# Optimization experiments

Hardware: AMD Instinct MI355X
Metric: run time of the kernel (lower is better)

The kernel has to match this reference:

```python
import jax, jax.numpy as jnp
import numpy as np

B, PS, ENC = 64, 14, 2048
DEC, ATT, EMB = 512, 512, 512
V, L = 10000, 52


def setup_inputs() -> dict:
    key = jax.random.key(0)
    ks = jax.random.split(key, 24)
    rn = lambda k, shp, s=0.02: (jax.random.normal(k, shp) * s).astype(jnp.float32)
    lengths = jax.random.randint(ks[2], (B, 1), 2, L + 1)
    lengths = lengths.at[0, 0].set(L)  # ensure max(decode_lengths) == L-1 (static)
    return {
        "encoder_output": jax.random.normal(ks[0], (B, PS, PS, ENC), jnp.float32),
        "encoded_captions": jax.random.randint(ks[1], (B, L), 0, V),
        "caption_lengths": lengths,
        # embedding (torch init: uniform(-0.1, 0.1))
        "emb_W": jax.random.uniform(ks[3], (V, EMB), jnp.float32, -0.1, 0.1),
        # attention linears
        "att_enc_W": rn(ks[4], (ENC, ATT)), "att_enc_b": jnp.zeros((ATT,), jnp.float32),
        "att_dec_W": rn(ks[5], (DEC, ATT)), "att_dec_b": jnp.zeros((ATT,), jnp.float32),
        "att_full_w": rn(ks[6], (ATT,)), "att_full_b": jnp.zeros((), jnp.float32),
        # LSTMCell(input = EMB + ENC, hidden = DEC)
        "lstm_Wih": rn(ks[7], (4 * DEC, EMB + ENC)), "lstm_Whh": rn(ks[8], (4 * DEC, DEC)),
        "lstm_bih": jnp.zeros((4 * DEC,), jnp.float32), "lstm_bhh": jnp.zeros((4 * DEC,), jnp.float32),
        # init_h / init_c / f_beta / fc
        "initH_W": rn(ks[9], (ENC, DEC)), "initH_b": jnp.zeros((DEC,), jnp.float32),
        "initC_W": rn(ks[10], (ENC, DEC)), "initC_b": jnp.zeros((DEC,), jnp.float32),
        "fbeta_W": rn(ks[11], (DEC, ENC)), "fbeta_b": jnp.zeros((ENC,), jnp.float32),
        "fc_W": jax.random.uniform(ks[12], (DEC, V), jnp.float32, -0.1, 0.1),
        "fc_b": jnp.zeros((V,), jnp.float32),
    }


def reference(encoder_output, encoded_captions, caption_lengths,
              emb_W, att_enc_W, att_enc_b, att_dec_W, att_dec_b,
              att_full_w, att_full_b, lstm_Wih, lstm_Whh, lstm_bih, lstm_bhh,
              initH_W, initH_b, initC_W, initC_b, fbeta_W, fbeta_b, fc_W, fc_b):
    b = encoder_output.shape[0]
    lengths = caption_lengths[:, 0]
    order = jnp.argsort(-lengths)                     # sort descending (sort_idx)
    lengths = lengths[order]
    enc = encoder_output.reshape(b, -1, ENC)[order]   # [B, P, ENC]
    caps = encoded_captions[order]                    # [B, L]
    emb = emb_W[caps]                                 # [B, L, EMB]
    dec_len = lengths - 1                             # decode lengths
    T = caps.shape[1] - 1                             # static max(decode_lengths)

    mean_enc = enc.mean(axis=1)
    h0 = mean_enc @ initH_W + initH_b
    c0 = mean_enc @ initC_W + initC_b
    # precompute encoder half of the attention MLP once
    att1 = jnp.einsum('bpe,ea->bpa', enc, att_enc_W) + att_enc_b  # [B, P, ATT]

    def step(carry, t):
        h, c = carry
        mask = (t < dec_len)[:, None]                 # rows still decoding
        att2 = h @ att_dec_W + att_dec_b              # [B, ATT]
        e = jax.nn.relu(att1 + att2[:, None, :]) @ att_full_w + att_full_b  # [B, P]
        alpha = jax.nn.softmax(e, axis=-1)
        awe = jnp.einsum('bp,bpe->be', alpha, enc)    # attention-weighted encoding
        gate = jax.nn.sigmoid(h @ fbeta_W + fbeta_b)
        x = jnp.concatenate([emb[:, t, :], gate * awe], axis=1)
        gates = x @ lstm_Wih.T + lstm_bih + h @ lstm_Whh.T + lstm_bhh
        i, f, g, o = jnp.split(gates, 4, axis=1)
        c_new = jax.nn.sigmoid(f) * c + jax.nn.sigmoid(i) * jnp.tanh(g)
        h_new = jax.nn.sigmoid(o) * jnp.tanh(c_new)
        pred = h_new @ fc_W + fc_b                    # dropout p=0 -> identity
        h = jnp.where(mask, h_new, h)
        c = jnp.where(mask, c_new, c)
        return (h, c), (jnp.where(mask, pred, 0.0), jnp.where(mask, alpha, 0.0))

    _, (preds, alphas) = jax.lax.scan(step, (h0, c0), jnp.arange(T))
    preds = jnp.transpose(preds, (1, 0, 2))           # [B, T, V]
    alphas = jnp.transpose(alphas, (1, 0, 2))         # [B, T, P]
    return preds, caps, dec_len, alphas, order
```

## Files before the change

### kernel.cpp

```cpp
#include <hip/hip_runtime.h>
#include <math.h>

#define BATCH 64
#define PIX   196
#define ENCD  2048
#define DECD  512
#define ATTD  512
#define EMBD  512
#define VOC   10000
#define LCAP  52
#define TSTEPS 51
#define XHDIM 3072

typedef __bf16 bfv8 __attribute__((ext_vector_type(8)));
typedef float  fv4  __attribute__((ext_vector_type(4)));

__device__ __forceinline__ float bf2f(unsigned short u) {
    union { unsigned int i; float f; } x; x.i = ((unsigned int)u) << 16; return x.f;
}
__device__ __forceinline__ unsigned short f2bf(float f) {
    union { float f; unsigned int i; } x; x.f = f;
    unsigned int r = x.i + 0x7fffu + ((x.i >> 16) & 1u);
    return (unsigned short)(r >> 16);
}

__global__ void k_setup(const int* caps, const int* lens,
                        int* order, int* declen,
                        float* caps_out, float* declen_out, float* order_out) {
    __shared__ int sl[64];
    __shared__ int so[64];
    int tid = threadIdx.x;
    sl[tid] = lens[tid];
    __syncthreads();
    int li = sl[tid];
    int pos = 0;
    for (int j = 0; j < 64; ++j) {
        int lj = sl[j];
        if (lj > li || (lj == li && j < tid)) pos++;
    }
    so[pos] = tid;
    __syncthreads();
    int ob = so[tid];
    order[tid] = ob;
    int dl = sl[ob] - 1;
    declen[tid] = dl;
    order_out[tid] = (float)ob;
    declen_out[tid] = (float)dl;
    for (int l = 0; l < LCAP; ++l)
        caps_out[tid * LCAP + l] = (float)caps[ob * LCAP + l];
}

__global__ void k_emb_all(const float* embW, const int* caps, const int* order,
                          unsigned short* emb_all, unsigned short* xh) {
    int b = blockIdx.x, t = blockIdx.y, tid = threadIdx.x;
    int tok = caps[order[b] * LCAP + t];
    float4 v = *(const float4*)(embW + (size_t)tok * EMBD + tid * 4);
    ushort4 o;
    o.x = f2bf(v.x); o.y = f2bf(v.y); o.z = f2bf(v.z); o.w = f2bf(v.w);
    *(ushort4*)(emb_all + ((size_t)t * 64 + b) * EMBD + tid * 4) = o;
    if (t == 0)
        *(ushort4*)(xh + (size_t)b * XHDIM + tid * 4) = o;
}

__global__ __launch_bounds__(256) void k_cvt_T(const float* src, unsigned short* dst,
                                               int R, int C) {
    __shared__ float tile[64][65];
    int c0 = blockIdx.x * 64, r0 = blockIdx.y * 64, tid = threadIdx.x;
    for (int idx = tid; idx < 4096; idx += 256) {
        int r = idx >> 6, c = idx & 63;
        float v = 0.f;
        if (r0 + r < R && c0 + c < C) v = src[(size_t)(r0 + r) * C + c0 + c];
        tile[r][c] = v;
    }
    __syncthreads();
    for (int idx = tid; idx < 4096; idx += 256) {
        int c = idx >> 6, r = idx & 63;
        if (c0 + c < C && r0 + r < R)
            dst[(size_t)(c0 + c) * R + r0 + r] = f2bf(tile[r][c]);
    }
}

__global__ void k_cvt_comb(const float* Wih, const float* Whh, unsigned short* W) {
    int j = blockIdx.x, tid = threadIdx.x;
    for (int k = tid * 4; k < XHDIM; k += 1024) {
        const float* src = (k < 2560) ? (Wih + (size_t)j * 2560 + k)
                                      : (Whh + (size_t)j * 512 + (k - 2560));
        float4 v = *(const float4*)src;
        ushort4 o;
        o.x = f2bf(v.x); o.y = f2bf(v.y); o.z = f2bf(v.z); o.w = f2bf(v.w);
        *(ushort4*)(W + (size_t)j * XHDIM + k) = o;
    }
}

__global__ void k_cvt_enc(const float* enc, const int* order, unsigned short* enc_bf) {
    int b = blockIdx.x, p = blockIdx.y, tid = threadIdx.x;
    const float* src = enc + ((size_t)order[b] * PIX + p) * ENCD + tid * 8;
    float4 v0 = *(const float4*)src;
    float4 v1 = *(const float4*)(src + 4);
    unsigned short o[8];
    o[0] = f2bf(v0.x); o[1] = f2bf(v0.y); o[2] = f2bf(v0.z); o[3] = f2bf(v0.w);
    o[4] = f2bf(v1.x); o[5] = f2bf(v1.y); o[6] = f2bf(v1.z); o[7] = f2bf(v1.w);
    *(uint4*)(enc_bf + ((size_t)b * PIX + p) * ENCD + tid * 8) = *(uint4*)o;
}

__global__ void k_mean(const float* enc, const int* order, float* meanv) {
    int b = blockIdx.x;
    int col = blockIdx.y * 256 + threadIdx.x;
    int ob = order[b];
    const float* base = enc + (size_t)ob * PIX * ENCD + col;
    float acc = 0.f;
    for (int p = 0; p < PIX; ++p) acc += base[(size_t)p * ENCD];
    meanv[b * ENCD + col] = acc * (1.0f / (float)PIX);
}

__global__ __launch_bounds__(256) void k_h0c0(const float* meanv,
                                              const float* WH, const float* bH,
                                              const float* WC, const float* bC,
                                              float* h, float* c, unsigned short* xh) {
    __shared__ float As[64 * 33];
    __shared__ float Bs[32 * 65];
    int nt = blockIdx.x, tid = threadIdx.x;
    const float* W; const float* bias; float* out; int j0; bool isH;
    if (nt < 8) { W = WH; bias = bH; out = h; j0 = nt * 64; isH = true; }
    else        { W = WC; bias = bC; out = c; j0 = (nt - 8) * 64; isH = false; }
    float acc[4][4] = {};
    int tr = tid & 15, tc = tid >> 4;
    for (int k0 = 0; k0 < ENCD; k0 += 32) {
        for (int idx = tid; idx < 512; idx += 256) {
            int rl = idx >> 3, k4 = (idx & 7) << 2;
            float4 v = *(const float4*)(meanv + (size_t)rl * ENCD + k0 + k4);
            float* d = As + rl * 33 + k4;
            d[0] = v.x; d[1] = v.y; d[2] = v.z; d[3] = v.w;
        }
        for (int idx = tid; idx < 512; idx += 256) {
            int k = idx >> 4, j4 = (idx & 15) << 2;
            float4 v = *(const float4*)(W + (size_t)(k0 + k) * DECD + j0 + j4);
            float* d = Bs + k * 65 + j4;
            d[0] = v.x; d[1] = v.y; d[2] = v.z; d[3] = v.w;
        }
        __syncthreads();
        for (int kk = 0; kk < 32; ++kk) {
            float a[4], bb[4];
            for (int i = 0; i < 4; ++i) a[i] = As[(tr * 4 + i) * 33 + kk];
            for (int i = 0; i < 4; ++i) bb[i] = Bs[kk * 65 + tc * 4 + i];
            for (int i = 0; i < 4; ++i)
                for (int j2 = 0; j2 < 4; ++j2) acc[i][j2] += a[i] * bb[j2];
        }
        __syncthreads();
    }
    for (int i = 0; i < 4; ++i)
        for (int j2 = 0; j2 < 4; ++j2) {
            int r = tr * 4 + i, j = j0 + tc * 4 + j2;
            float v = acc[i][j2] + bias[j];
            out[r * DECD + j] = v;
            if (isH) xh[(size_t)r * XHDIM + 2560 + j] = f2bf(v);
        }
}

__device__ __forceinline__ void mm64_core(
    const unsigned short* __restrict__ A, int lda,
    const unsigned short* __restrict__ Bt, int ldb,
    int K, int nvalid,
    unsigned short* __restrict__ As, unsigned short* __restrict__ Bs,
    fv4* __restrict__ acc)
{
    const int tid = threadIdx.x;
    const int lane = tid & 63;
    const int w = tid >> 6, wr = w >> 1, wc = w & 1;
    const int lr = lane & 15, lk = (lane >> 4) << 3;
    const int sr = tid >> 2, sc = (tid & 3) << 3;
    const unsigned short* ap = A + (size_t)sr * lda + sc;
    const unsigned short* bp = Bt + (size_t)sr * ldb + sc;
    const bool bok = sr < nvalid;
    unsigned short* aw = As + sr * 40 + sc;
    unsigned short* bw = Bs + sr * 40 + sc;
    const unsigned short* a0p = As + (wr * 32 + lr) * 40 + lk;
    const unsigned short* a1p = a0p + 16 * 40;
    const unsigned short* b0p = Bs + (wc * 32 + lr) * 40 + lk;
    const unsigned short* b1p = b0p + 16 * 40;

    uint4 av = *(const uint4*)ap;
    uint4 bv;
    if (bok) bv = *(const uint4*)bp; else { bv.x = bv.y = bv.z = bv.w = 0u; }

    for (int k0 = 0; k0 < K; k0 += 32) {
        __syncthreads();
        *(uint4*)aw = av;
        *(uint4*)bw = bv;
        if (k0 + 32 < K) {
            av = *(const uint4*)(ap + k0 + 32);
            if (bok) bv = *(const uint4*)(bp + k0 + 32);
            else { bv.x = bv.y = bv.z = bv.w = 0u; }
        }
        __syncthreads();
        bfv8 a0 = *(const bfv8*)a0p;
        bfv8 a1 = *(const bfv8*)a1p;
        bfv8 b0 = *(const bfv8*)b0p;
        bfv8 b1 = *(const bfv8*)b1p;
        acc[0] = __builtin_amdgcn_mfma_f32_16x16x32_bf16(a0, b0, acc[0], 0, 0, 0);
        acc[1] = __builtin_amdgcn_mfma_f32_16x16x32_bf16(a0, b1, acc[1], 0, 0, 0);
        acc[2] = __builtin_amdgcn_mfma_f32_16x16x32_bf16(a1, b0, acc[2], 0, 0, 0);
        acc[3] = __builtin_amdgcn_mfma_f32_16x16x32_bf16(a1, b1, acc[3], 0, 0, 0);
    }
}

#define MM64_DECL_EPI \
    int lane = threadIdx.x & 63; int w = threadIdx.x >> 6; \
    int wr = w >> 1, wc = w & 1; \
    int rg = (lane >> 4) << 2, cg = lane & 15;

__global__ __launch_bounds__(256) void k_att1_mfma(
    const unsigned short* __restrict__ enc_bf, const unsigned short* __restrict__ WaeT,
    const float* __restrict__ bias, unsigned short* __restrict__ att1bf) {
    __shared__ __align__(16) unsigned short As[64 * 40];
    __shared__ __align__(16) unsigned short Bs[64 * 40];
    int r0 = blockIdx.x * 64, a0 = blockIdx.y * 64;
    fv4 acc[4];
    acc[0] = (fv4)0.f; acc[1] = (fv4)0.f; acc[2] = (fv4)0.f; acc[3] = (fv4)0.f;
    mm64_core(enc_bf + (size_t)r0 * ENCD, ENCD,
              WaeT + (size_t)a0 * ENCD, ENCD, ENCD, 64, As, Bs, acc);
    MM64_DECL_EPI
    #pragma unroll
    for (int m = 0; m < 2; ++m)
      #pragma unroll
      for (int n = 0; n < 2; ++n)
        #pragma unroll
        for (int r = 0; r < 4; ++r) {
            int row = r0 + wr * 32 + m * 16 + rg + r;
            int col = a0 + wc * 32 + n * 16 + cg;
            att1bf[(size_t)row * ATTD + col] = f2bf(acc[m * 2 + n][r] + bias[col]);
        }
}

__global__ __launch_bounds__(256) void k_att2gate_mfma(
    const unsigned short* __restrict__ xh, const unsigned short* __restrict__ W2T,
    const float* __restrict__ bad, const float* __restrict__ bfb,
    float* __restrict__ att2, float* __restrict__ gate) {
    __shared__ __align__(16) unsigned short As[64 * 40];
    __shared__ __align__(16) unsigned short Bs[64 * 40];
    int j0 = blockIdx.x * 64;
    fv4 acc[4];
    acc[0] = (fv4)0.f; acc[1] = (fv4)0.f; acc[2] = (fv4)0.f; acc[3] = (fv4)0.f;
    mm64_core(xh + 2560, XHDIM, W2T + (size_t)j0 * DECD, DECD, DECD, 64, As, Bs, acc);
    MM64_DECL_EPI
    #pragma unroll
    for (int m = 0; m < 2; ++m)
      #pragma unroll
      for (int n = 0; n < 2; ++n)
        #pragma unroll
        for (int r = 0; r < 4; ++r) {
            int row = wr * 32 + m * 16 + rg + r;
            int jg = j0 + wc * 32 + n * 16 + cg;
            float v = acc[m * 2 + n][r];
            if (jg < ATTD) {
                att2[row * ATTD + jg] = v + bad[jg];
            } else {
                int jj = jg - ATTD;
                gate[row * ENCD + jj] = 1.f / (1.f + expf(-(v + bfb[jj])));
            }
        }
}

__global__ __launch_bounds__(256) void k_gates_mfma(
    const unsigned short* __restrict__ xh, const unsigned short* __restrict__ W,
    float* __restrict__ partial) {
    __shared__ __align__(16) unsigned short As[64 * 40];
    __shared__ __align__(16) unsigned short Bs[64 * 40];
    int jt = blockIdx.x, kc = blockIdx.y;
    fv4 acc[4];
    acc[0] = (fv4)0.f; acc[1] = (fv4)0.f; acc[2] = (fv4)0.f; acc[3] = (fv4)0.f;
    mm64_core(xh + kc * 512, XHDIM,
              W + (size_t)jt * 64 * XHDIM + kc * 512, XHDIM, 512, 64, As, Bs, acc);
    float* out = partial + (size_t)kc * (64 * 2048);
    MM64_DECL_EPI
    #pragma unroll
    for (int m = 0; m < 2; ++m)
      #pragma unroll
      for (int n = 0; n < 2; ++n)
        #pragma unroll
        for (int r = 0; r < 4; ++r) {
            int row = wr * 32 + m * 16 + rg + r;
            int col = jt * 64 + wc * 32 + n * 16 + cg;
            out[row * 2048 + col] = acc[m * 2 + n][r];
        }
}

__global__ __launch_bounds__(256) void k_fc_mfma(
    const unsigned short* __restrict__ hallbf, const unsigned short* __restrict__ WfcT,
    const float* __restrict__ bias, const int* __restrict__ declen,
    float* __restrict__ preds) {
    __shared__ __align__(16) unsigned short As[64 * 40];
    __shared__ __align__(16) unsigned short Bs[64 * 40];
    int v0 = blockIdx.x * 64, tt = blockIdx.y;
    int nv = VOC - v0; if (nv > 64) nv = 64;
    fv4 acc[4];
    acc[0] = (fv4)0.f; acc[1] = (fv4)0.f; acc[2] = (fv4)0.f; acc[3] = (fv4)0.f;
    mm64_core(hallbf + (size_t)tt * 64 * DECD, DECD,
              WfcT + (size_t)v0 * DECD, DECD, DECD, nv, As, Bs, acc);
    MM64_DECL_EPI
    #pragma unroll
    for (int m = 0; m < 2; ++m)
      #pragma unroll
      for (int n = 0; n < 2; ++n)
        #pragma unroll
        for (int r = 0; r < 4; ++r) {
            int b = wr * 32 + m * 16 + rg + r;
            int v = v0 + wc * 32 + n * 16 + cg;
            if (v < VOC) {
                bool mask = tt < declen[b];
                preds[((size_t)b * TSTEPS + tt) * VOC + v] =
                    mask ? (acc[m * 2 + n][r] + bias[v]) : 0.f;
            }
        }
}

__global__ void k_e(const unsigned short* att1bf, const float* att2,
                    const float* wfull, const float* bfull, float* e) {
    __shared__ float a2s[512];
    __shared__ float wfs[512];
    int b = blockIdx.x, tid = threadIdx.x;
    a2s[tid] = att2[b * ATTD + tid];
    a2s[tid + 256] = att2[b * ATTD + tid + 256];
    wfs[tid] = wfull[tid];
    wfs[tid + 256] = wfull[tid + 256];
    __syncthreads();
    int p = blockIdx.y * 4 + (tid >> 6);
    int lane = tid & 63;
    uint4 v = *(const uint4*)(att1bf + ((size_t)b * PIX + p) * ATTD + lane * 8);
    const unsigned short* us = (const unsigned short*)&v;
    float acc = 0.f;
    for (int jj = 0; jj < 8; ++jj) {
        int a = lane * 8 + jj;
        float x = bf2f(us[jj]) + a2s[a];
        x = fmaxf(x, 0.f);
        acc += x * wfs[a];
    }
    for (int off = 32; off; off >>= 1) acc += __shfl_down(acc, off);
    if (lane == 0) e[b * PIX + p] = acc + bfull[0];
}

__global__ void k_awe(const float* e, const unsigned short* enc_bf,
                      const float* gate, const int* declen,
                      unsigned short* xh, float* alphas_out, int t) {
    __shared__ float sal[256];
    __shared__ float sred[256];
    __shared__ float sacc[2048];
    int b = blockIdx.x, ch = blockIdx.y, tid = threadIdx.x;
    float ev = (tid < PIX) ? e[b * PIX + tid] : -1e30f;
    sred[tid] = ev; __syncthreads();
    for (int s = 128; s; s >>= 1) { if (tid < s) sred[tid] = fmaxf(sred[tid], sred[tid + s]); __syncthreads(); }
    float m = sred[0]; __syncthreads();
    float pv = (tid < PIX) ? expf(ev - m) : 0.f;
    sred[tid] = pv; __syncthreads();
    for (int s = 128; s; s >>= 1) { if (tid < s) sred[tid] += sred[tid + s]; __syncthreads(); }
    float inv = 1.f / sred[0];
    float al = pv * inv;
    sal[tid] = al;
    if (ch == 0 && tid < PIX) {
        bool mask = t < declen[b];
        alphas_out[((size_t)b * TSTEPS + t) * PIX + tid] = mask ? al : 0.f;
    }
    __syncthreads();
    int g = tid & 31, pp = tid >> 5;
    float acc[8] = {};
    const unsigned short* base = enc_bf + (size_t)b * PIX * ENCD + ch * 256 + g * 8;
    for (int p = pp; p < PIX; p += 8) {
        uint4 v = *(const uint4*)(base + (size_t)p * ENCD);
        const unsigned short* us = (const unsigned short*)&v;
        float a = sal[p];
        for (int jj = 0; jj < 8; ++jj) acc[jj] += a * bf2f(us[jj]);
    }
    for (int jj = 0; jj < 8; ++jj) sacc[pp * 256 + g * 8 + jj] = acc[jj];
    __syncthreads();
    float s = 0.f;
    for (int q = 0; q < 8; ++q) s += sacc[q * 256 + tid];
    int col = ch * 256 + tid;
    xh[(size_t)b * XHDIM + EMBD + col] = f2bf(gate[b * ENCD + col] * s);
}

__global__ void k_update(const float* partial, const float* bih, const float* bhh,
                         const int* declen, float* h, float* c,
                         unsigned short* hallbf, const unsigned short* emb_all,
                         unsigned short* xh, int t) {
    int b = blockIdx.x, d = threadIdx.x;
    float g[4];
    for (int q = 0; q < 4; ++q) {
        int j = q * 512 + d;
        float acc = bih[j] + bhh[j];
        for (int kc = 0; kc < 6; ++kc) acc += partial[(size_t)kc * 131072 + b * 2048 + j];
        g[q] = acc;
    }
    float si = 1.f / (1.f + expf(-g[0]));
    float sf = 1.f / (1.f + expf(-g[1]));
    float gg = tanhf(g[2]);
    float so = 1.f / (1.f + expf(-g[3]));
    float c_old = c[b * DECD + d], h_old = h[b * DECD + d];
    float c_new = sf * c_old + si * gg;
    float h_new = so * tanhf(c_new);
    bool mask = t < declen[b];
    float h_keep = mask ? h_new : h_old;
    h[b * DECD + d] = h_keep;
    c[b * DECD + d] = mask ? c_new : c_old;
    xh[(size_t)b * XHDIM + 2560 + d] = f2bf(h_keep);
    hallbf[((size_t)t * 64 + b) * DECD + d] = f2bf(h_new);
    if (t + 1 < TSTEPS)
        xh[(size_t)b * XHDIM + d] = emb_all[((size_t)(t + 1) * 64 + b) * EMBD + d];
}

extern "C" void kernel_launch(void* const* d_in, const int* in_sizes, int n_in,
                              void* d_out, int out_size, void* d_ws, size_t ws_size,
                              hipStream_t stream) {
    const float* enc      = (const float*)d_in[0];
    const int*   caps     = (const int*)d_in[1];
    const int*   lens     = (const int*)d_in[2];
    const float* embW     = (const float*)d_in[3];
    const float* att_enc_W = (const float*)d_in[4];
    const float* att_enc_b = (const float*)d_in[5];
    const float* att_dec_W = (const float*)d_in[6];
    const float* att_dec_b = (const float*)d_in[7];
    const float* att_full_w = (const float*)d_in[8];
    const float* att_full_b = (const float*)d_in[9];
    const float* lstm_Wih = (const float*)d_in[10];
    const float* lstm_Whh = (const float*)d_in[11];
    const float* lstm_bih = (const float*)d_in[12];
    const float* lstm_bhh = (const float*)d_in[13];
    const float* initH_W  = (const float*)d_in[14];
    const float* initH_b  = (const float*)d_in[15];
    const float* initC_W  = (const float*)d_in[16];
    const float* initC_b  = (const float*)d_in[17];
    const float* fbeta_W  = (const float*)d_in[18];
    const float* fbeta_b  = (const float*)d_in[19];
    const float* fc_W     = (const float*)d_in[20];
    const float* fc_b     = (const float*)d_in[21];

    float* o = (float*)d_out;
    float* preds_out  = o;
    float* caps_out   = o + (size_t)BATCH * TSTEPS * VOC;
    float* declen_out = caps_out + (size_t)BATCH * LCAP;
    float* order_out  = declen_out + BATCH;
    float* alphas_out = order_out + BATCH;

    char* wsb = (char*)d_ws;
    int* i_order  = (int*)wsb;
    int* i_declen = i_order + 64;
    float* f = (float*)(wsb + 512);
    float* f_h     = f;  f += (size_t)BATCH * DECD;
    float* f_c     = f;  f += (size_t)BATCH * DECD;
    float* f_att2  = f;  f += (size_t)BATCH * ATTD;
    float* f_gate  = f;  f += (size_t)BATCH * ENCD;
    float* f_e     = f;  f += (size_t)BATCH * PIX;
    f = (float*)(((uintptr_t)f + 255) & ~(uintptr_t)255);
    float* f_part  = f;  f += (size_t)6 * BATCH * 2048;
    float* f_mean = f_part;
    unsigned short* WaeT = (unsigned short*)(f_part + (size_t)BATCH * ENCD);
    f = (float*)(((uintptr_t)f + 255) & ~(uintptr_t)255);
    unsigned short* bf = (unsigned short*)f;
    unsigned short* xh_bf    = bf;  bf += (size_t)BATCH * XHDIM;
    unsigned short* att1_bf  = bf;  bf += (size_t)BATCH * PIX * ATTD;
    unsigned short* Wcomb_bf = bf;  bf += (size_t)2048 * XHDIM;
    unsigned short* W2T      = bf;  bf += (size_t)(ATTD + ENCD) * DECD;
    unsigned short* WfcT     = bf;  bf += (size_t)VOC * DECD;
    unsigned short* emb_all  = bf;  bf += (size_t)TSTEPS * BATCH * EMBD;
    unsigned short* hall_bf  = bf;  bf += (size_t)TSTEPS * BATCH * DECD;
    bf = (unsigned short*)(((uintptr_t)bf + 255) & ~(uintptr_t)255);
    unsigned short* enc_bf   = bf;  bf += (size_t)BATCH * PIX * ENCD;

    k_setup<<<1, 64, 0, stream>>>(caps, lens, i_order, i_declen,
                                  caps_out, declen_out, order_out);
    k_emb_all<<<dim3(BATCH, TSTEPS), 128, 0, stream>>>(embW, caps, i_order,
                                                       emb_all, xh_bf);
    k_cvt_comb<<<2048, 256, 0, stream>>>(lstm_Wih, lstm_Whh, Wcomb_bf);
    k_cvt_enc<<<dim3(BATCH, PIX), 256, 0, stream>>>(enc, i_order, enc_bf);
    k_cvt_T<<<dim3(8, 8),   256, 0, stream>>>(att_dec_W, W2T, DECD, ATTD);
    k_cvt_T<<<dim3(32, 8),  256, 0, stream>>>(fbeta_W, W2T + (size_t)ATTD * DECD, DECD, ENCD);
    k_cvt_T<<<dim3(8, 32),  256, 0, stream>>>(att_enc_W, WaeT, ENCD, ATTD);
    k_cvt_T<<<dim3(157, 8), 256, 0, stream>>>(fc_W, WfcT, DECD, VOC);
    k_mean<<<dim3(BATCH, ENCD / 256), 256, 0, stream>>>(enc, i_order, f_mean);
    k_h0c0<<<16, 256, 0, stream>>>(f_mean, initH_W, initH_b, initC_W, initC_b,
                                   f_h, f_c, xh_bf);
    k_att1_mfma<<<dim3(PIX, ATTD / 64), 256, 0, stream>>>(enc_bf, WaeT,
                                                          att_enc_b, att1_bf);

    for (int t = 0; t < TSTEPS; ++t) {
        k_att2gate_mfma<<<40, 256, 0, stream>>>(xh_bf, W2T, att_dec_b, fbeta_b,
                                                f_att2, f_gate);
        k_e<<<dim3(BATCH, 49), 256, 0, stream>>>(att1_bf, f_att2, att_full_w,
                                                 att_full_b, f_e);
        k_awe<<<dim3(BATCH, 8), 256, 0, stream>>>(f_e, enc_bf, f_gate, i_declen,
                                                  xh_bf, alphas_out, t);
        k_gates_mfma<<<dim3(32, 6), 256, 0, stream>>>(xh_bf, Wcomb_bf, f_part);
        k_update<<<BATCH, DECD, 0, stream>>>(f_part, lstm_bih, lstm_bhh, i_declen,
                                             f_h, f_c, hall_bf, emb_all, xh_bf, t);
    }

    k_fc_mfma<<<dim3((VOC + 63) / 64, TSTEPS), 256, 0, stream>>>(hall_bf, WfcT,
                                                                 fc_b, i_declen,
                                                                 preds_out);
}
```

Measured before the change: 2.674 ms.

## Fuse per-timestep decoder kernels into one persistent cooperative kernel with grid syncs

Replaces the five kernel launches per timestep with a single persistent cooperative kernel of 256 blocks that runs all 51 steps, separating the phases with grid.sync(). The h-dependent slice of the LSTM gate matmul is computed alongside the att2/gate matmul, so the later gate matmul only covers the remaining five K-chunks. The aim is to remove roughly 255 launch gaps and their tail effects. In exchange it adds grid-wide barrier costs and fixes each phase to a set work split, and it falls back to the old launch loop if the cooperative launch fails.

```diff
diff --git a/kernel.cpp b/kernel.cpp
--- a/kernel.cpp
+++ b/kernel.cpp
@@ -1,5 +1,8 @@
 #include <hip/hip_runtime.h>
+#include <hip/hip_cooperative_groups.h>
 #include <math.h>
+
+namespace cg = cooperative_groups;
 
 #define BATCH 64
 #define PIX   196
@@ -229,59 +232,6 @@
             int row = r0 + wr * 32 + m * 16 + rg + r;
             int col = a0 + wc * 32 + n * 16 + cg;
             att1bf[(size_t)row * ATTD + col] = f2bf(acc[m * 2 + n][r] + bias[col]);
-        }
-}
-
-__global__ __launch_bounds__(256) void k_att2gate_mfma(
-    const unsigned short* __restrict__ xh, const unsigned short* __restrict__ W2T,
-    const float* __restrict__ bad, const float* __restrict__ bfb,
-    float* __restrict__ att2, float* __restrict__ gate) {
-    __shared__ __align__(16) unsigned short As[64 * 40];
-    __shared__ __align__(16) unsigned short Bs[64 * 40];
-    int j0 = blockIdx.x * 64;
-    fv4 acc[4];
-    acc[0] = (fv4)0.f; acc[1] = (fv4)0.f; acc[2] = (fv4)0.f; acc[3] = (fv4)0.f;
-    mm64_core(xh + 2560, XHDIM, W2T + (size_t)j0 * DECD, DECD, DECD, 64, As, Bs, acc);
-    MM64_DECL_EPI
-    #pragma unroll
-    for (int m = 0; m < 2; ++m)
-      #pragma unroll
-      for (int n = 0; n < 2; ++n)
-        #pragma unroll
-        for (int r = 0; r < 4; ++r) {
-            int row = wr * 32 + m * 16 + rg + r;
-            int jg = j0 + wc * 32 + n * 16 + cg;
-            float v = acc[m * 2 + n][r];
-            if (jg < ATTD) {
-                att2[row * ATTD + jg] = v + bad[jg];
-            } else {
-                int jj = jg - ATTD;
-                gate[row * ENCD + jj] = 1.f / (1.f + expf(-(v + bfb[jj])));
-            }
-        }
-}
-
-__global__ __launch_bounds__(256) void k_gates_mfma(
-    const unsigned short* __restrict__ xh, const unsigned short* __restrict__ W,
-    float* __restrict__ partial) {
-    __shared__ __align__(16) unsigned short As[64 * 40];
-    __shared__ __align__(16) unsigned short Bs[64 * 40];
-    int jt = blockIdx.x, kc = blockIdx.y;
-    fv4 acc[4];
-    acc[0] = (fv4)0.f; acc[1] = (fv4)0.f; acc[2] = (fv4)0.f; acc[3] = (fv4)0.f;
-    mm64_core(xh + kc * 512, XHDIM,
-              W + (size_t)jt * 64 * XHDIM + kc * 512, XHDIM, 512, 64, As, Bs, acc);
-    float* out = partial + (size_t)kc * (64 * 2048);
-    MM64_DECL_EPI
-    #pragma unroll
-    for (int m = 0; m < 2; ++m)
-      #pragma unroll
-      for (int n = 0; n < 2; ++n)
-        #pragma unroll
-        for (int r = 0; r < 4; ++r) {
-            int row = wr * 32 + m * 16 + rg + r;
-            int col = jt * 64 + wc * 32 + n * 16 + cg;
-            out[row * 2048 + col] = acc[m * 2 + n][r];
         }
 }
 
@@ -314,6 +264,253 @@
         }
 }
 
+struct LoopArgs {
+    const unsigned short* W2T;
+    const unsigned short* Wcomb;
+    const unsigned short* att1;
+    const unsigned short* enc;
+    const unsigned short* emb_all;
+    unsigned short* xh;
+    unsigned short* hall;
+    const float* bad; const float* bfb;
+    const float* wfull; const float* bfull;
+    const float* bih; const float* bhh;
+    float* att2; float* gate; float* e; float* part;
+    float* h; float* c; float* alphas;
+    const int* declen;
+};
+
+__global__ __launch_bounds__(256) void k_loop(LoopArgs a) {
+    cg::grid_group grid = cg::this_grid();
+    __shared__ __align__(16) unsigned short As[64 * 40];
+    __shared__ __align__(16) unsigned short Bs[64 * 40];
+    __shared__ float sal[256];
+    __shared__ float sred[256];
+    __shared__ float sacc[2048];
+    const int bid = blockIdx.x, tid = threadIdx.x;
+
+    for (int t = 0; t < TSTEPS; ++t) {
+        if (bid < 40) {
+            int j0 = bid * 64;
+            fv4 acc[4];
+            acc[0] = (fv4)0.f; acc[1] = (fv4)0.f; acc[2] = (fv4)0.f; acc[3] = (fv4)0.f;
+            mm64_core(a.xh + 2560, XHDIM, a.W2T + (size_t)j0 * DECD, DECD,
+                      DECD, 64, As, Bs, acc);
+            MM64_DECL_EPI
+            #pragma unroll
+            for (int m = 0; m < 2; ++m)
+              #pragma unroll
+              for (int n = 0; n < 2; ++n)
+                #pragma unroll
+                for (int r = 0; r < 4; ++r) {
+                    int row = wr * 32 + m * 16 + rg + r;
+                    int jg = j0 + wc * 32 + n * 16 + cg;
+                    float v = acc[m * 2 + n][r];
+                    if (jg < ATTD) {
+                        a.att2[row * ATTD + jg] = v + a.bad[jg];
+                    } else {
+                        int jj = jg - ATTD;
+                        a.gate[row * ENCD + jj] = 1.f / (1.f + expf(-(v + a.bfb[jj])));
+                    }
+                }
+        } else if (bid < 72) {
+            int jt = bid - 40;
+            fv4 acc[4];
+            acc[0] = (fv4)0.f; acc[1] = (fv4)0.f; acc[2] = (fv4)0.f; acc[3] = (fv4)0.f;
+            mm64_core(a.xh + 2560, XHDIM,
+                      a.Wcomb + (size_t)jt * 64 * XHDIM + 2560, XHDIM,
+                      512, 64, As, Bs, acc);
+            float* out = a.part + (size_t)5 * (64 * 2048);
+            MM64_DECL_EPI
+            #pragma unroll
+            for (int m = 0; m < 2; ++m)
+              #pragma unroll
+              for (int n = 0; n < 2; ++n)
+                #pragma unroll
+                for (int r = 0; r < 4; ++r) {
+                    int row = wr * 32 + m * 16 + rg + r;
+                    int col = jt * 64 + wc * 32 + n * 16 + cg;
+                    out[row * 2048 + col] = acc[m * 2 + n][r];
+                }
+        }
+        grid.sync();
+
+        {
+            int lane = tid & 63;
+            int gw = bid * 4 + (tid >> 6);
+            const float* a2base = a.att2;
+            for (int u = gw; u < BATCH * PIX; u += 1024) {
+                int b = u / PIX, p = u % PIX;
+                uint4 v = *(const uint4*)(a.att1 + ((size_t)b * PIX + p) * ATTD + lane * 8);
+                const unsigned short* us = (const unsigned short*)&v;
+                const float* a2 = a2base + b * ATTD + lane * 8;
+                float4 a2a = *(const float4*)a2;
+                float4 a2b = *(const float4*)(a2 + 4);
+                const float* wf = a.wfull + lane * 8;
+                float4 wfa = *(const float4*)wf;
+                float4 wfb = *(const float4*)(wf + 4);
+                float accv;
+                accv  = fmaxf(bf2f(us[0]) + a2a.x, 0.f) * wfa.x;
+                accv += fmaxf(bf2f(us[1]) + a2a.y, 0.f) * wfa.y;
+                accv += fmaxf(bf2f(us[2]) + a2a.z, 0.f) * wfa.z;
+                accv += fmaxf(bf2f(us[3]) + a2a.w, 0.f) * wfa.w;
+                accv += fmaxf(bf2f(us[4]) + a2b.x, 0.f) * wfb.x;
+                accv += fmaxf(bf2f(us[5]) + a2b.y, 0.f) * wfb.y;
+                accv += fmaxf(bf2f(us[6]) + a2b.z, 0.f) * wfb.z;
+                accv += fmaxf(bf2f(us[7]) + a2b.w, 0.f) * wfb.w;
+                for (int off = 32; off; off >>= 1) accv += __shfl_down(accv, off);
+                if (lane == 0) a.e[b * PIX + p] = accv + a.bfull[0];
+            }
+        }
+        grid.sync();
+
+        {
+            int b = bid >> 2, pair = bid & 3;
+            float ev = (tid < PIX) ? a.e[b * PIX + tid] : -1e30f;
+            sred[tid] = ev; __syncthreads();
+            for (int s = 128; s; s >>= 1) {
+                if (tid < s) sred[tid] = fmaxf(sred[tid], sred[tid + s]);
+                __syncthreads();
+            }
+            float m = sred[0]; __syncthreads();
+            float pv = (tid < PIX) ? expf(ev - m) : 0.f;
+            sred[tid] = pv; __syncthreads();
+            for (int s = 128; s; s >>= 1) {
+                if (tid < s) sred[tid] += sred[tid + s];
+                __syncthreads();
+            }
+            float inv = 1.f / sred[0];
+            float al = pv * inv;
+            sal[tid] = al;
+            if (pair == 0 && tid < PIX) {
+                bool mask = t < a.declen[b];
+                a.alphas[((size_t)b * TSTEPS + t) * PIX + tid] = mask ? al : 0.f;
+            }
+            __syncthreads();
+            int g = tid & 31, pp = tid >> 5;
+            #pragma unroll
+            for (int cc = 0; cc < 2; ++cc) {
+                int ch = pair * 2 + cc;
+                float acc[8] = {};
+                const unsigned short* base =
+                    a.enc + (size_t)b * PIX * ENCD + ch * 256 + g * 8;
+                for (int p = pp; p < PIX; p += 8) {
+                    uint4 v = *(const uint4*)(base + (size_t)p * ENCD);
+                    const unsigned short* us = (const unsigned short*)&v;
+                    float av = sal[p];
+                    #pragma unroll
+                    for (int jj = 0; jj < 8; ++jj) acc[jj] += av * bf2f(us[jj]);
+                }
+                #pragma unroll
+                for (int jj = 0; jj < 8; ++jj) sacc[pp * 256 + g * 8 + jj] = acc[jj];
+                __syncthreads();
+                float s = 0.f;
+                #pragma unroll
+                for (int q = 0; q < 8; ++q) s += sacc[q * 256 + tid];
+                int col = ch * 256 + tid;
+                a.xh[(size_t)b * XHDIM + EMBD + col] = f2bf(a.gate[b * ENCD + col] * s);
+                __syncthreads();
+            }
+        }
+        grid.sync();
+
+        if (bid < 160) {
+            int jt = bid / 5, kc = bid % 5;
+            fv4 acc[4];
+            acc[0] = (fv4)0.f; acc[1] = (fv4)0.f; acc[2] = (fv4)0.f; acc[3] = (fv4)0.f;
+            mm64_core(a.xh + kc * 512, XHDIM,
+                      a.Wcomb + (size_t)jt * 64 * XHDIM + kc * 512, XHDIM,
+                      512, 64, As, Bs, acc);
+            float* out = a.part + (size_t)kc * (64 * 2048);
+            MM64_DECL_EPI
+            #pragma unroll
+            for (int m = 0; m < 2; ++m)
+              #pragma unroll
+              for (int n = 0; n < 2; ++n)
+                #pragma unroll
+                for (int r = 0; r < 4; ++r) {
+                    int row = wr * 32 + m * 16 + rg + r;
+                    int col = jt * 64 + wc * 32 + n * 16 + cg;
+                    out[row * 2048 + col] = acc[m * 2 + n][r];
+                }
+        }
+        grid.sync();
+
+        if (bid < 128) {
+            int b = bid >> 1, d = (bid & 1) * 256 + tid;
+            float gv[4];
+            #pragma unroll
+            for (int q = 0; q < 4; ++q) {
+                int j = q * 512 + d;
+                float acc = a.bih[j] + a.bhh[j];
+                #pragma unroll
+                for (int kc = 0; kc < 6; ++kc)
+                    acc += a.part[(size_t)kc * 131072 + b * 2048 + j];
+                gv[q] = acc;
+            }
+            float si = 1.f / (1.f + expf(-gv[0]));
+            float sf = 1.f / (1.f + expf(-gv[1]));
+            float gg = tanhf(gv[2]);
+            float so = 1.f / (1.f + expf(-gv[3]));
+            float c_old = a.c[b * DECD + d], h_old = a.h[b * DECD + d];
+            float c_new = sf * c_old + si * gg;
+            float h_new = so * tanhf(c_new);
+            bool mask = t < a.declen[b];
+            float h_keep = mask ? h_new : h_old;
+            a.h[b * DECD + d] = h_keep;
+            a.c[b * DECD + d] = mask ? c_new : c_old;
+            a.xh[(size_t)b * XHDIM + 2560 + d] = f2bf(h_keep);
+            a.hall[((size_t)t * 64 + b) * DECD + d] = f2bf(h_new);
+            if (t + 1 < TSTEPS)
+                a.xh[(size_t)b * XHDIM + d] = a.emb_all[((size_t)(t + 1) * 64 + b) * EMBD + d];
+        }
+        grid.sync();
+    }
+}
+
+__global__ __launch_bounds__(256) void k_att2gate_mfma(
+    const unsigned short* __restrict__ xh, const unsigned short* __restrict__ W2T,
+    const float* __restrict__ bad, const float* __restrict__ bfb,
+    float* __restrict__ att2, float* __restrict__ gate) {
+    __shared__ __align__(16) unsigned short As[64 * 40];
+    __shared__ __align__(16) unsigned short Bs[64 * 40];
+    int j0 = blockIdx.x * 64;
+    fv4 acc[4];
+    acc[0] = (fv4)0.f; acc[1] = (fv4)0.f; acc[2] = (fv4)0.f; acc[3] = (fv4)0.f;
+    mm64_core(xh + 2560, XHDIM, W2T + (size_t)j0 * DECD, DECD, DECD, 64, As, Bs, acc);
+    MM64_DECL_EPI
+    for (int m = 0; m < 2; ++m)
+      for (int n = 0; n < 2; ++n)
+        for (int r = 0; r < 4; ++r) {
+            int row = wr * 32 + m * 16 + rg + r;
+            int jg = j0 + wc * 32 + n * 16 + cg;
+            float v = acc[m * 2 + n][r];
+            if (jg < ATTD) att2[row * ATTD + jg] = v + bad[jg];
+            else { int jj = jg - ATTD; gate[row * ENCD + jj] = 1.f / (1.f + expf(-(v + bfb[jj]))); }
+        }
+}
+
+__global__ __launch_bounds__(256) void k_gates_mfma(
+    const unsigned short* __restrict__ xh, const unsigned short* __restrict__ W,
+    float* __restrict__ partial) {
+    __shared__ __align__(16) unsigned short As[64 * 40];
+    __shared__ __align__(16) unsigned short Bs[64 * 40];
+    int jt = blockIdx.x, kc = blockIdx.y;
+    fv4 acc[4];
+    acc[0] = (fv4)0.f; acc[1] = (fv4)0.f; acc[2] = (fv4)0.f; acc[3] = (fv4)0.f;
+    mm64_core(xh + kc * 512, XHDIM,
+              W + (size_t)jt * 64 * XHDIM + kc * 512, XHDIM, 512, 64, As, Bs, acc);
+    float* out = partial + (size_t)kc * (64 * 2048);
+    MM64_DECL_EPI
+    for (int m = 0; m < 2; ++m)
+      for (int n = 0; n < 2; ++n)
+        for (int r = 0; r < 4; ++r) {
+            int row = wr * 32 + m * 16 + rg + r;
+            int col = jt * 64 + wc * 32 + n * 16 + cg;
+            out[row * 2048 + col] = acc[m * 2 + n][r];
+        }
+}
+
 __global__ void k_e(const unsigned short* att1bf, const float* att2,
                     const float* wfull, const float* bfull, float* e) {
     __shared__ float a2s[512];
@@ -481,16 +678,37 @@
     k_att1_mfma<<<dim3(PIX, ATTD / 64), 256, 0, stream>>>(enc_bf, WaeT,
                                                           att_enc_b, att1_bf);
 
-    for (int t = 0; t < TSTEPS; ++t) {
-        k_att2gate_mfma<<<40, 256, 0, stream>>>(xh_bf, W2T, att_dec_b, fbeta_b,
-                                                f_att2, f_gate);
-        k_e<<<dim3(BATCH, 49), 256, 0, stream>>>(att1_bf, f_att2, att_full_w,
-                                                 att_full_b, f_e);
-        k_awe<<<dim3(BATCH, 8), 256, 0, stream>>>(f_e, enc_bf, f_gate, i_declen,
-                                                  xh_bf, alphas_out, t);
-        k_gates_mfma<<<dim3(32, 6), 256, 0, stream>>>(xh_bf, Wcomb_bf, f_part);
-        k_update<<<BATCH, DECD, 0, stream>>>(f_part, lstm_bih, lstm_bhh, i_declen,
-                                             f_h, f_c, hall_bf, emb_all, xh_bf, t);
+    int maxb = 0;
+    hipError_t qerr = hipOccupancyMaxActiveBlocksPerMultiprocessor(
+        &maxb, (const void*)k_loop, 256, 0);
+    bool coop_ok = (qerr == hipSuccess) && (maxb >= 1);
+
+    if (coop_ok) {
+        LoopArgs la;
+        la.W2T = W2T; la.Wcomb = Wcomb_bf; la.att1 = att1_bf; la.enc = enc_bf;
+        la.emb_all = emb_all; la.xh = xh_bf; la.hall = hall_bf;
+        la.bad = att_dec_b; la.bfb = fbeta_b; la.wfull = att_full_w;
+        la.bfull = att_full_b; la.bih = lstm_bih; la.bhh = lstm_bhh;
+        la.att2 = f_att2; la.gate = f_gate; la.e = f_e; la.part = f_part;
+        la.h = f_h; la.c = f_c; la.alphas = alphas_out; la.declen = i_declen;
+        void* kargs[] = { (void*)&la };
+        hipError_t lerr = hipLaunchCooperativeKernel(
+            (const void*)k_loop, dim3(256), dim3(256), kargs, 0, stream);
+        coop_ok = (lerr == hipSuccess);
+    }
+
+    if (!coop_ok) {
+        for (int t = 0; t < TSTEPS; ++t) {
+            k_att2gate_mfma<<<40, 256, 0, stream>>>(xh_bf, W2T, att_dec_b, fbeta_b,
+                                                    f_att2, f_gate);
+            k_e<<<dim3(BATCH, 49), 256, 0, stream>>>(att1_bf, f_att2, att_full_w,
+                                                     att_full_b, f_e);
+            k_awe<<<dim3(BATCH, 8), 256, 0, stream>>>(f_e, enc_bf, f_gate, i_declen,
+                                                      xh_bf, alphas_out, t);
+            k_gates_mfma<<<dim3(32, 6), 256, 0, stream>>>(xh_bf, Wcomb_bf, f_part);
+            k_update<<<BATCH, DECD, 0, stream>>>(f_part, lstm_bih, lstm_bhh, i_declen,
+                                                 f_h, f_c, hall_bf, emb_all, xh_bf, t);
+        }
     }
 
     k_fc_mfma<<<dim3((VOC + 63) / 64, TSTEPS), 256, 0, stream>>>(hall_bf, WfcT,
```

Measured after the change: 2.705 ms. Within noise of the previous version (+1.2%).

## Fuse per-step decoder kernels into two and overlap FC projection with recurrence

Applied to the files above, without the earlier changes.

Collapses the five per-timestep kernels into two. The first computes att2 and the gate with per-wave dot products, then the attention scores, softmax and weighted encoding in one block per (batch, quarter). The second runs the full-K LSTM gate GEMM, with Wcomb rows permuted so each tile holds all four gates for 16 hidden units, and applies the cell update in the epilogue. Its spare blocks compute the vocabulary projection for the previous step, so the separate FC GEMM overlaps the serial recurrence. This cuts launch count and global round-trips for partial sums, at the cost of a serial K=3072 loop in only 32 blocks and redundant att2 recomputation across the four blocks per batch row.

```diff
diff --git a/kernel.cpp b/kernel.cpp
--- a/kernel.cpp
+++ b/kernel.cpp
@@ -82,13 +82,15 @@
 
 __global__ void k_cvt_comb(const float* Wih, const float* Whh, unsigned short* W) {
     int j = blockIdx.x, tid = threadIdx.x;
+    int q = j >> 9, d = j & 511;
+    int nr = ((d >> 4) << 6) + (q << 4) + (d & 15);
     for (int k = tid * 4; k < XHDIM; k += 1024) {
         const float* src = (k < 2560) ? (Wih + (size_t)j * 2560 + k)
                                       : (Whh + (size_t)j * 512 + (k - 2560));
         float4 v = *(const float4*)src;
         ushort4 o;
         o.x = f2bf(v.x); o.y = f2bf(v.y); o.z = f2bf(v.z); o.w = f2bf(v.w);
-        *(ushort4*)(W + (size_t)j * XHDIM + k) = o;
+        *(ushort4*)(W + (size_t)nr * XHDIM + k) = o;
     }
 }
 
@@ -232,66 +234,12 @@
         }
 }
 
-__global__ __launch_bounds__(256) void k_att2gate_mfma(
-    const unsigned short* __restrict__ xh, const unsigned short* __restrict__ W2T,
-    const float* __restrict__ bad, const float* __restrict__ bfb,
-    float* __restrict__ att2, float* __restrict__ gate) {
-    __shared__ __align__(16) unsigned short As[64 * 40];
-    __shared__ __align__(16) unsigned short Bs[64 * 40];
-    int j0 = blockIdx.x * 64;
-    fv4 acc[4];
-    acc[0] = (fv4)0.f; acc[1] = (fv4)0.f; acc[2] = (fv4)0.f; acc[3] = (fv4)0.f;
-    mm64_core(xh + 2560, XHDIM, W2T + (size_t)j0 * DECD, DECD, DECD, 64, As, Bs, acc);
-    MM64_DECL_EPI
-    #pragma unroll
-    for (int m = 0; m < 2; ++m)
-      #pragma unroll
-      for (int n = 0; n < 2; ++n)
-        #pragma unroll
-        for (int r = 0; r < 4; ++r) {
-            int row = wr * 32 + m * 16 + rg + r;
-            int jg = j0 + wc * 32 + n * 16 + cg;
-            float v = acc[m * 2 + n][r];
-            if (jg < ATTD) {
-                att2[row * ATTD + jg] = v + bad[jg];
-            } else {
-                int jj = jg - ATTD;
-                gate[row * ENCD + jj] = 1.f / (1.f + expf(-(v + bfb[jj])));
-            }
-        }
-}
-
-__global__ __launch_bounds__(256) void k_gates_mfma(
-    const unsigned short* __restrict__ xh, const unsigned short* __restrict__ W,
-    float* __restrict__ partial) {
-    __shared__ __align__(16) unsigned short As[64 * 40];
-    __shared__ __align__(16) unsigned short Bs[64 * 40];
-    int jt = blockIdx.x, kc = blockIdx.y;
-    fv4 acc[4];
-    acc[0] = (fv4)0.f; acc[1] = (fv4)0.f; acc[2] = (fv4)0.f; acc[3] = (fv4)0.f;
-    mm64_core(xh + kc * 512, XHDIM,
-              W + (size_t)jt * 64 * XHDIM + kc * 512, XHDIM, 512, 64, As, Bs, acc);
-    float* out = partial + (size_t)kc * (64 * 2048);
-    MM64_DECL_EPI
-    #pragma unroll
-    for (int m = 0; m < 2; ++m)
-      #pragma unroll
-      for (int n = 0; n < 2; ++n)
-        #pragma unroll
-        for (int r = 0; r < 4; ++r) {
-            int row = wr * 32 + m * 16 + rg + r;
-            int col = jt * 64 + wc * 32 + n * 16 + cg;
-            out[row * 2048 + col] = acc[m * 2 + n][r];
-        }
-}
-
-__global__ __launch_bounds__(256) void k_fc_mfma(
+__device__ __forceinline__ void fc_tile(
     const unsigned short* __restrict__ hallbf, const unsigned short* __restrict__ WfcT,
     const float* __restrict__ bias, const int* __restrict__ declen,
-    float* __restrict__ preds) {
-    __shared__ __align__(16) unsigned short As[64 * 40];
-    __shared__ __align__(16) unsigned short Bs[64 * 40];
-    int v0 = blockIdx.x * 64, tt = blockIdx.y;
+    float* __restrict__ preds, int vt, int tt,
+    unsigned short* __restrict__ As, unsigned short* __restrict__ Bs) {
+    int v0 = vt * 64;
     int nv = VOC - v0; if (nv > 64) nv = 64;
     fv4 acc[4];
     acc[0] = (fv4)0.f; acc[1] = (fv4)0.f; acc[2] = (fv4)0.f; acc[3] = (fv4)0.f;
@@ -314,97 +262,206 @@
         }
 }
 
-__global__ void k_e(const unsigned short* att1bf, const float* att2,
-                    const float* wfull, const float* bfull, float* e) {
+__global__ __launch_bounds__(256) void k_fc_one(
+    const unsigned short* __restrict__ hallbf, const unsigned short* __restrict__ WfcT,
+    const float* __restrict__ bias, const int* __restrict__ declen,
+    float* __restrict__ preds, int tt) {
+    __shared__ __align__(16) unsigned short As[64 * 40];
+    __shared__ __align__(16) unsigned short Bs[64 * 40];
+    fc_tile(hallbf, WfcT, bias, declen, preds, blockIdx.x, tt, As, Bs);
+}
+
+__global__ __launch_bounds__(512) void k_step1(
+    const unsigned short* __restrict__ W2T,
+    const unsigned short* __restrict__ att1,
+    const unsigned short* __restrict__ enc,
+    const unsigned short* __restrict__ emb_all,
+    const float* __restrict__ h,
+    const float* __restrict__ bad, const float* __restrict__ bfb,
+    const float* __restrict__ wfull, const float* __restrict__ bfull,
+    const int* __restrict__ declen,
+    unsigned short* __restrict__ xh, float* __restrict__ alphas, int t)
+{
+    __shared__ float hs[512];
     __shared__ float a2s[512];
-    __shared__ float wfs[512];
-    int b = blockIdx.x, tid = threadIdx.x;
-    a2s[tid] = att2[b * ATTD + tid];
-    a2s[tid + 256] = att2[b * ATTD + tid + 256];
-    wfs[tid] = wfull[tid];
-    wfs[tid + 256] = wfull[tid + 256];
-    __syncthreads();
-    int p = blockIdx.y * 4 + (tid >> 6);
-    int lane = tid & 63;
-    uint4 v = *(const uint4*)(att1bf + ((size_t)b * PIX + p) * ATTD + lane * 8);
-    const unsigned short* us = (const unsigned short*)&v;
-    float acc = 0.f;
-    for (int jj = 0; jj < 8; ++jj) {
-        int a = lane * 8 + jj;
-        float x = bf2f(us[jj]) + a2s[a];
-        x = fmaxf(x, 0.f);
-        acc += x * wfs[a];
-    }
-    for (int off = 32; off; off >>= 1) acc += __shfl_down(acc, off);
-    if (lane == 0) e[b * PIX + p] = acc + bfull[0];
-}
-
-__global__ void k_awe(const float* e, const unsigned short* enc_bf,
-                      const float* gate, const int* declen,
-                      unsigned short* xh, float* alphas_out, int t) {
+    __shared__ float sgate[512];
+    __shared__ float se[256];
+    __shared__ float sred[256];
     __shared__ float sal[256];
-    __shared__ float sred[256];
-    __shared__ float sacc[2048];
-    int b = blockIdx.x, ch = blockIdx.y, tid = threadIdx.x;
-    float ev = (tid < PIX) ? e[b * PIX + tid] : -1e30f;
-    sred[tid] = ev; __syncthreads();
-    for (int s = 128; s; s >>= 1) { if (tid < s) sred[tid] = fmaxf(sred[tid], sred[tid + s]); __syncthreads(); }
-    float m = sred[0]; __syncthreads();
+    __shared__ float sacc[8][512];
+    const int bid = blockIdx.x;
+    const int b = bid >> 2, s = bid & 3;
+    const int tid = threadIdx.x;
+    const int lane = tid & 63, wv = tid >> 6;
+
+    if (tid < 128)
+        *(float4*)(hs + tid * 4) = *(const float4*)(h + b * DECD + tid * 4);
+    __syncthreads();
+
+    float hreg[8];
+    #pragma unroll
+    for (int j = 0; j < 8; ++j) hreg[j] = hs[lane * 8 + j];
+
+    for (int cc = 0; cc < 64; ++cc) {
+        int c = wv * 64 + cc;
+        uint4 wrow = *(const uint4*)(W2T + (size_t)c * DECD + lane * 8);
+        const unsigned short* us = (const unsigned short*)&wrow;
+        float d = bf2f(us[0]) * hreg[0] + bf2f(us[1]) * hreg[1]
+                + bf2f(us[2]) * hreg[2] + bf2f(us[3]) * hreg[3]
+                + bf2f(us[4]) * hreg[4] + bf2f(us[5]) * hreg[5]
+                + bf2f(us[6]) * hreg[6] + bf2f(us[7]) * hreg[7];
+        for (int off = 32; off; off >>= 1) d += __shfl_down(d, off);
+        if (lane == 0) a2s[c] = d + bad[c];
+    }
+    for (int cc = 0; cc < 64; ++cc) {
+        int cl = wv * 64 + cc;
+        int row = ATTD + s * 512 + cl;
+        uint4 wrow = *(const uint4*)(W2T + (size_t)row * DECD + lane * 8);
+        const unsigned short* us = (const unsigned short*)&wrow;
+        float d = bf2f(us[0]) * hreg[0] + bf2f(us[1]) * hreg[1]
+                + bf2f(us[2]) * hreg[2] + bf2f(us[3]) * hreg[3]
+                + bf2f(us[4]) * hreg[4] + bf2f(us[5]) * hreg[5]
+                + bf2f(us[6]) * hreg[6] + bf2f(us[7]) * hreg[7];
+        for (int off = 32; off; off >>= 1) d += __shfl_down(d, off);
+        if (lane == 0) sgate[cl] = 1.f / (1.f + expf(-(d + bfb[s * 512 + cl])));
+    }
+    __syncthreads();
+
+    {
+        float4 a2a = *(const float4*)(a2s + lane * 8);
+        float4 a2b = *(const float4*)(a2s + lane * 8 + 4);
+        float4 wfa = *(const float4*)(wfull + lane * 8);
+        float4 wfb = *(const float4*)(wfull + lane * 8 + 4);
+        float bf0 = bfull[0];
+        for (int p = wv; p < PIX; p += 8) {
+            uint4 v = *(const uint4*)(att1 + ((size_t)b * PIX + p) * ATTD + lane * 8);
+            const unsigned short* us = (const unsigned short*)&v;
+            float accv;
+            accv  = fmaxf(bf2f(us[0]) + a2a.x, 0.f) * wfa.x;
+            accv += fmaxf(bf2f(us[1]) + a2a.y, 0.f) * wfa.y;
+            accv += fmaxf(bf2f(us[2]) + a2a.z, 0.f) * wfa.z;
+            accv += fmaxf(bf2f(us[3]) + a2a.w, 0.f) * wfa.w;
+            accv += fmaxf(bf2f(us[4]) + a2b.x, 0.f) * wfb.x;
+            accv += fmaxf(bf2f(us[5]) + a2b.y, 0.f) * wfb.y;
+            accv += fmaxf(bf2f(us[6]) + a2b.z, 0.f) * wfb.z;
+            accv += fmaxf(bf2f(us[7]) + a2b.w, 0.f) * wfb.w;
+            for (int off = 32; off; off >>= 1) accv += __shfl_down(accv, off);
+            if (lane == 0) se[p] = accv + bf0;
+        }
+    }
+    __syncthreads();
+
+    float ev = (tid < PIX) ? se[tid] : -1e30f;
+    if (tid < 256) sred[tid] = ev;
+    __syncthreads();
+    for (int ss = 128; ss; ss >>= 1) {
+        if (tid < ss) sred[tid] = fmaxf(sred[tid], sred[tid + ss]);
+        __syncthreads();
+    }
+    float m = sred[0];
+    __syncthreads();
     float pv = (tid < PIX) ? expf(ev - m) : 0.f;
-    sred[tid] = pv; __syncthreads();
-    for (int s = 128; s; s >>= 1) { if (tid < s) sred[tid] += sred[tid + s]; __syncthreads(); }
+    if (tid < 256) sred[tid] = pv;
+    __syncthreads();
+    for (int ss = 128; ss; ss >>= 1) {
+        if (tid < ss) sred[tid] += sred[tid + ss];
+        __syncthreads();
+    }
     float inv = 1.f / sred[0];
     float al = pv * inv;
-    sal[tid] = al;
-    if (ch == 0 && tid < PIX) {
-        bool mask = t < declen[b];
-        alphas_out[((size_t)b * TSTEPS + t) * PIX + tid] = mask ? al : 0.f;
-    }
-    __syncthreads();
-    int g = tid & 31, pp = tid >> 5;
-    float acc[8] = {};
-    const unsigned short* base = enc_bf + (size_t)b * PIX * ENCD + ch * 256 + g * 8;
-    for (int p = pp; p < PIX; p += 8) {
-        uint4 v = *(const uint4*)(base + (size_t)p * ENCD);
-        const unsigned short* us = (const unsigned short*)&v;
-        float a = sal[p];
-        for (int jj = 0; jj < 8; ++jj) acc[jj] += a * bf2f(us[jj]);
-    }
-    for (int jj = 0; jj < 8; ++jj) sacc[pp * 256 + g * 8 + jj] = acc[jj];
-    __syncthreads();
-    float s = 0.f;
-    for (int q = 0; q < 8; ++q) s += sacc[q * 256 + tid];
-    int col = ch * 256 + tid;
-    xh[(size_t)b * XHDIM + EMBD + col] = f2bf(gate[b * ENCD + col] * s);
-}
-
-__global__ void k_update(const float* partial, const float* bih, const float* bhh,
-                         const int* declen, float* h, float* c,
-                         unsigned short* hallbf, const unsigned short* emb_all,
-                         unsigned short* xh, int t) {
-    int b = blockIdx.x, d = threadIdx.x;
-    float g[4];
-    for (int q = 0; q < 4; ++q) {
-        int j = q * 512 + d;
-        float acc = bih[j] + bhh[j];
-        for (int kc = 0; kc < 6; ++kc) acc += partial[(size_t)kc * 131072 + b * 2048 + j];
-        g[q] = acc;
-    }
-    float si = 1.f / (1.f + expf(-g[0]));
-    float sf = 1.f / (1.f + expf(-g[1]));
-    float gg = tanhf(g[2]);
-    float so = 1.f / (1.f + expf(-g[3]));
-    float c_old = c[b * DECD + d], h_old = h[b * DECD + d];
-    float c_new = sf * c_old + si * gg;
-    float h_new = so * tanhf(c_new);
-    bool mask = t < declen[b];
-    float h_keep = mask ? h_new : h_old;
-    h[b * DECD + d] = h_keep;
-    c[b * DECD + d] = mask ? c_new : c_old;
-    xh[(size_t)b * XHDIM + 2560 + d] = f2bf(h_keep);
-    hallbf[((size_t)t * 64 + b) * DECD + d] = f2bf(h_new);
-    if (t + 1 < TSTEPS)
-        xh[(size_t)b * XHDIM + d] = emb_all[((size_t)(t + 1) * 64 + b) * EMBD + d];
+    if (tid < PIX) {
+        sal[tid] = al;
+        if (s == 0) {
+            bool mask = t < declen[b];
+            alphas[((size_t)b * TSTEPS + t) * PIX + tid] = mask ? al : 0.f;
+        }
+    }
+    if (s == 0 && tid < 64)
+        *(uint4*)(xh + (size_t)b * XHDIM + tid * 8) =
+            *(const uint4*)(emb_all + ((size_t)t * 64 + b) * EMBD + tid * 8);
+    __syncthreads();
+
+    {
+        int g = tid & 63, pp = tid >> 6;
+        float acc[8] = {};
+        const unsigned short* base =
+            enc + (size_t)b * PIX * ENCD + s * 512 + g * 8;
+        for (int p = pp; p < PIX; p += 8) {
+            uint4 v = *(const uint4*)(base + (size_t)p * ENCD);
+            const unsigned short* us = (const unsigned short*)&v;
+            float av = sal[p];
+            #pragma unroll
+            for (int jj = 0; jj < 8; ++jj) acc[jj] += av * bf2f(us[jj]);
+        }
+        #pragma unroll
+        for (int jj = 0; jj < 8; ++jj) sacc[pp][g * 8 + jj] = acc[jj];
+        __syncthreads();
+        float sum = 0.f;
+        #pragma unroll
+        for (int q = 0; q < 8; ++q) sum += sacc[q][tid];
+        xh[(size_t)b * XHDIM + EMBD + s * 512 + tid] = f2bf(sgate[tid] * sum);
+    }
+}
+
+__global__ __launch_bounds__(256) void k_step2(
+    const unsigned short* __restrict__ xh, const unsigned short* __restrict__ Wcomb,
+    const unsigned short* __restrict__ WfcT, const float* __restrict__ fcb,
+    const float* __restrict__ bih, const float* __restrict__ bhh,
+    const int* __restrict__ declen,
+    float* __restrict__ h, float* __restrict__ c,
+    unsigned short* __restrict__ hall, unsigned short* __restrict__ xh_out,
+    float* __restrict__ preds, int t)
+{
+    __shared__ __align__(16) unsigned short As[64 * 40];
+    __shared__ __align__(16) unsigned short Bs[64 * 40];
+    __shared__ float gacc[64][65];
+    const int bid = blockIdx.x, tid = threadIdx.x;
+
+    if (bid < 32) {
+        int jt = bid;
+        fv4 acc[4];
+        acc[0] = (fv4)0.f; acc[1] = (fv4)0.f; acc[2] = (fv4)0.f; acc[3] = (fv4)0.f;
+        mm64_core(xh, XHDIM, Wcomb + (size_t)jt * 64 * XHDIM, XHDIM,
+                  XHDIM, 64, As, Bs, acc);
+        {
+            MM64_DECL_EPI
+            #pragma unroll
+            for (int m = 0; m < 2; ++m)
+              #pragma unroll
+              for (int n = 0; n < 2; ++n)
+                #pragma unroll
+                for (int r = 0; r < 4; ++r)
+                    gacc[wr * 32 + m * 16 + rg + r][wc * 32 + n * 16 + cg] =
+                        acc[m * 2 + n][r];
+        }
+        __syncthreads();
+        #pragma unroll
+        for (int it = 0; it < 4; ++it) {
+            int idx = it * 256 + tid;
+            int b = idx >> 4, dd = idx & 15;
+            int d = jt * 16 + dd;
+            float gv[4];
+            #pragma unroll
+            for (int q = 0; q < 4; ++q)
+                gv[q] = gacc[b][q * 16 + dd] + bih[q * 512 + d] + bhh[q * 512 + d];
+            float si = 1.f / (1.f + expf(-gv[0]));
+            float sf = 1.f / (1.f + expf(-gv[1]));
+            float gg = tanhf(gv[2]);
+            float so = 1.f / (1.f + expf(-gv[3]));
+            float c_old = c[b * DECD + d], h_old = h[b * DECD + d];
+            float c_new = sf * c_old + si * gg;
+            float h_new = so * tanhf(c_new);
+            bool mask = t < declen[b];
+            float h_keep = mask ? h_new : h_old;
+            h[b * DECD + d] = h_keep;
+            c[b * DECD + d] = mask ? c_new : c_old;
+            xh_out[(size_t)b * XHDIM + 2560 + d] = f2bf(h_keep);
+            hall[((size_t)t * 64 + b) * DECD + d] = f2bf(h_new);
+        }
+    } else {
+        if (t > 0)
+            fc_tile(hall, WfcT, fcb, declen, preds, bid - 32, t - 1, As, Bs);
+    }
 }
 
 extern "C" void kernel_launch(void* const* d_in, const int* in_sizes, int n_in,
@@ -446,9 +503,6 @@
     float* f = (float*)(wsb + 512);
     float* f_h     = f;  f += (size_t)BATCH * DECD;
     float* f_c     = f;  f += (size_t)BATCH * DECD;
-    float* f_att2  = f;  f += (size_t)BATCH * ATTD;
-    float* f_gate  = f;  f += (size_t)BATCH * ENCD;
-    float* f_e     = f;  f += (size_t)BATCH * PIX;
     f = (float*)(((uintptr_t)f + 255) & ~(uintptr_t)255);
     float* f_part  = f;  f += (size_t)6 * BATCH * 2048;
     float* f_mean = f_part;
@@ -482,18 +536,13 @@
                                                           att_enc_b, att1_bf);
 
     for (int t = 0; t < TSTEPS; ++t) {
-        k_att2gate_mfma<<<40, 256, 0, stream>>>(xh_bf, W2T, att_dec_b, fbeta_b,
-                                                f_att2, f_gate);
-        k_e<<<dim3(BATCH, 49), 256, 0, stream>>>(att1_bf, f_att2, att_full_w,
-                                                 att_full_b, f_e);
-        k_awe<<<dim3(BATCH, 8), 256, 0, stream>>>(f_e, enc_bf, f_gate, i_declen,
-                                                  xh_bf, alphas_out, t);
-        k_gates_mfma<<<dim3(32, 6), 256, 0, stream>>>(xh_bf, Wcomb_bf, f_part);
-        k_update<<<BATCH, DECD, 0, stream>>>(f_part, lstm_bih, lstm_bhh, i_declen,
-                                             f_h, f_c, hall_bf, emb_all, xh_bf, t);
-    }
-
-    k_fc_mfma<<<dim3((VOC + 63) / 64, TSTEPS), 256, 0, stream>>>(hall_bf, WfcT,
-                                                                 fc_b, i_declen,
-                                                                 preds_out);
-}
+        k_step1<<<256, 512, 0, stream>>>(W2T, att1_bf, enc_bf, emb_all, f_h,
+                                         att_dec_b, fbeta_b, att_full_w, att_full_b,
+                                         i_declen, xh_bf, alphas_out, t);
+        k_step2<<<189, 256, 0, stream>>>(xh_bf, Wcomb_bf, WfcT, fc_b,
+                                         lstm_bih, lstm_bhh, i_declen,
+                                         f_h, f_c, hall_bf, xh_bf, preds_out, t);
+    }
+    k_fc_one<<<157, 256, 0, stream>>>(hall_bf, WfcT, fc_b, i_declen,
+                                      preds_out, TSTEPS - 1);
+}
```

Measured after the change: 7.738 ms. +189.4%, slower.
